# Kernel optimization log

Hardware: AMD Instinct MI355X
Metric: run time of the kernel (lower is better)

## Reference

```python
import jax, jax.numpy as jnp
import numpy as np

N = 100000      # nodes
E = 1600000     # edges (before self-loops)
FIN = 128       # in_channels
HID = 16        # hidden_channels
H = 8           # heads (layer 1)
OUT = 64        # out_channels
LN_EPS = 1e-5


def setup_inputs() -> dict:
    key = jax.random.key(0)
    ks = jax.random.split(key, 24)
    def p(i, shape):
        return jax.random.normal(ks[i], shape, dtype=jnp.float32) * 0.05
    return {
        "x": jax.random.normal(ks[0], (N, FIN), dtype=jnp.float32),
        "edge_index": jax.random.randint(ks[1], (2, E), 0, N, dtype=jnp.int32),
        # GATv2 layer 1: in -> H*HID, concat
        "Wl1": p(2, (FIN, H * HID)), "bl1": p(3, (H * HID,)),
        "Wr1": p(4, (FIN, H * HID)), "br1": p(5, (H * HID,)),
        "att1": p(6, (H, HID)), "bias1": p(7, (H * HID,)),
        # GATv2 layer 2: H*HID -> HID, heads=1
        "Wl2": p(8, (H * HID, HID)), "bl2": p(9, (HID,)),
        "Wr2": p(10, (H * HID, HID)), "br2": p(11, (HID,)),
        "att2": p(12, (1, HID)), "bias2": p(13, (HID,)),
        # LayerNorms
        "ln1_g": jnp.ones((H * HID,), jnp.float32), "ln1_b": jnp.zeros((H * HID,), jnp.float32),
        "ln2_g": jnp.ones((HID,), jnp.float32), "ln2_b": jnp.zeros((HID,), jnp.float32),
        # residual / skip / output linears
        "res1_W": p(14, (FIN, H * HID)), "res1_b": p(15, (H * HID,)),
        "res2_W": p(16, (H * HID, HID)), "res2_b": p(17, (HID,)),
        "skip_W": p(18, (H * HID, HID)), "skip_b": p(19, (HID,)),
        "out_W": p(20, (HID, OUT)), "out_b": p(21, (OUT,)),
    }


def _layernorm(x, g, b):
    mu = jnp.mean(x, axis=-1, keepdims=True)
    var = jnp.mean((x - mu) ** 2, axis=-1, keepdims=True)
    return (x - mu) * jax.lax.rsqrt(var + LN_EPS) * g + b


def _gatv2(x, src, dst, Wl, bl, Wr, br, att, bias, concat):
    # PyG GATv2Conv (share_weights=False, eval mode): message from src j to dst i
    Hh, C = att.shape
    n = x.shape[0]
    xl = (x @ Wl + bl).reshape(n, Hh, C)   # source-side transform
    xr = (x @ Wr + br).reshape(n, Hh, C)   # target-side transform
    m = xl[src] + xr[dst]                  # [E, H, C]
    e = jax.nn.leaky_relu(m, 0.2)
    alpha = jnp.einsum('ehc,hc->eh', e, att)          # [E, H]
    amax = jax.ops.segment_max(alpha, dst, num_segments=n)
    alpha = jnp.exp(alpha - amax[dst])
    denom = jax.ops.segment_sum(alpha, dst, num_segments=n)
    alpha = alpha / (denom[dst] + 1e-16)
    out = jax.ops.segment_sum(xl[src] * alpha[:, :, None], dst, num_segments=n)  # [N, H, C]
    out = out.reshape(n, Hh * C) if concat else out.mean(axis=1)
    return out + bias


def reference(x, edge_index, Wl1, bl1, Wr1, br1, att1, bias1,
              Wl2, bl2, Wr2, br2, att2, bias2,
              ln1_g, ln1_b, ln2_g, ln2_b,
              res1_W, res1_b, res2_W, res2_b, skip_W, skip_b, out_W, out_b):
    n = x.shape[0]
    loops = jnp.arange(n, dtype=edge_index.dtype)
    src = jnp.concatenate([edge_index[0], loops])
    dst = jnp.concatenate([edge_index[1], loops])

    h = _gatv2(x, src, dst, Wl1, bl1, Wr1, br1, att1, bias1, concat=True)
    h = _layernorm(h, ln1_g, ln1_b)
    h = h + (x @ res1_W + res1_b)
    h = jax.nn.elu(h)            # dropout off in eval

    skip_in = h
    h2 = _gatv2(h, src, dst, Wl2, bl2, Wr2, br2, att2, bias2, concat=False)
    h2 = _layernorm(h2, ln2_g, ln2_b)
    h2 = h2 + (skip_in @ res2_W + res2_b)
    h2 = jax.nn.elu(h2)
    h2 = h2 + (skip_in @ skip_W + skip_b)
    return h2 @ out_W + out_b
```

## Files before the change

### kernel.cpp

```cpp
#include <hip/hip_runtime.h>

typedef __attribute__((ext_vector_type(8))) short bf16x8;
typedef __attribute__((ext_vector_type(4))) float f32x4;

__device__ __forceinline__ float bf2f(ushort u) {
  union { uint i; float f; } v; v.i = ((uint)u) << 16; return v.f;
}
__device__ __forceinline__ ushort f2bf(float f) {
  union { float f; uint i; } v; v.f = f;
  uint r = (v.i + 0x7FFFu + ((v.i >> 16) & 1u)) >> 16;
  return (ushort)r;
}
__device__ __forceinline__ float blo(uint u) { return __builtin_bit_cast(float, u << 16); }
__device__ __forceinline__ float bhi(uint u) { return __builtin_bit_cast(float, u & 0xffff0000u); }

template <int CTRL>
__device__ __forceinline__ float dppadd(float x) {
  union { float f; int i; } a, b;
  a.f = x;
  b.i = __builtin_amdgcn_update_dpp(0, a.i, CTRL, 0xF, 0xF, true);
  return a.f + b.f;
}
#define DPP_X1 0xB1
#define DPP_X2 0x4E
#define DPP_X7 0x141
#define DPP_XF 0x140


__global__ __launch_bounds__(256) void k_init(
    const float* __restrict__ Wl1, const float* __restrict__ bl1,
    const float* __restrict__ Wr1, const float* __restrict__ br1,
    const float* __restrict__ res1W, const float* __restrict__ res1b,
    const float* __restrict__ Wl2, const float* __restrict__ bl2,
    const float* __restrict__ Wr2, const float* __restrict__ br2,
    const float* __restrict__ res2W, const float* __restrict__ res2b,
    const float* __restrict__ skipW, const float* __restrict__ skipb,
    const float* __restrict__ att1, const float* __restrict__ att2,
    ushort* __restrict__ W1F, float* __restrict__ B1P,
    ushort* __restrict__ W2F, float* __restrict__ B2P,
    float* __restrict__ at6, float* __restrict__ at4, float* __restrict__ at2E,
    int* __restrict__ cnt, int N) {
  const float LOG2E = 1.4426950408889634f;
  int b = blockIdx.x, t = threadIdx.x;
  if (b < 227) {
    int tid = b * 256 + t;
    if (tid < 49152) {
      int j = tid & 7, l = (tid >> 3) & 63, ktile = (tid >> 9) & 3, ct = tid >> 11;
      int k = ktile * 32 + ((l >> 4) << 3) + j;
      int n = ct * 16 + (l & 15);
      int sel = n >> 7, jj = n & 127;
      const float* s = sel == 0 ? Wl1 : sel == 1 ? Wr1 : res1W;
      W1F[tid] = f2bf(s[k * 128 + jj]);
    } else if (tid < 57344) {
      int u = tid - 49152;
      int j = u & 7, l = (u >> 3) & 63, ktile = (u >> 9) & 3, ct = u >> 11;
      int k = ktile * 32 + ((l >> 4) << 3) + j;
      int n = ct * 16 + (l & 15);
      int sel = n >> 4, jj = n & 15;
      const float* s = sel == 0 ? Wl2 : sel == 1 ? Wr2 : sel == 2 ? res2W : skipW;
      W2F[u] = f2bf(s[k * 16 + jj]);
    } else if (tid < 57728) {
      int n = tid - 57344;
      int sel = n >> 7, jj = n & 127;
      const float* sb = sel == 0 ? bl1 : sel == 1 ? br1 : res1b;
      B1P[n] = sb[jj];
    } else if (tid < 57792) {
      int n = tid - 57728;
      int sel = n >> 4, jj = n & 15;
      const float* sb = sel == 0 ? bl2 : sel == 1 ? br2 : sel == 2 ? res2b : skipb;
      B2P[n] = sb[jj];
    } else if (tid < 57920) {
      int n = tid - 57792;
      at6[n] = att1[n] * 0.6f * LOG2E;
    } else if (tid < 58048) {
      int n = tid - 57920;
      at4[n] = att1[n] * 0.4f * LOG2E;
    } else if (tid < 58064) {
      int n = tid - 58048;
      at2E[n] = att2[n] * LOG2E;
    }
  } else {
    int idx = (b - 227) * 256 + t;
    if (idx < N) cnt[idx] = 0;
  }
}


__global__ __launch_bounds__(256) void k_hist(const int* __restrict__ ei, int* __restrict__ cnt, int E) {
  int e4 = (blockIdx.x * 256 + threadIdx.x) * 4;
  if (e4 + 3 < E) {
    int4 d = *(const int4*)&ei[E + e4];
    atomicAdd(&cnt[d.x], 1); atomicAdd(&cnt[d.y], 1);
    atomicAdd(&cnt[d.z], 1); atomicAdd(&cnt[d.w], 1);
  } else {
    for (int e = e4; e < E; ++e) atomicAdd(&cnt[ei[E + e]], 1);
  }
}


__global__ __launch_bounds__(256) void k_scan1(const int* __restrict__ cnt, int* __restrict__ partial, int n) {
  int i = blockIdx.x * 256 + threadIdx.x;
  int v = (i < n) ? cnt[i] : 0;
  #pragma unroll
  for (int m = 1; m < 64; m <<= 1) v += __shfl_xor(v, m);
  __shared__ int sm[4];
  if ((threadIdx.x & 63) == 0) sm[threadIdx.x >> 6] = v;
  __syncthreads();
  if (threadIdx.x == 0) partial[blockIdx.x] = sm[0] + sm[1] + sm[2] + sm[3];
}


__global__ __launch_bounds__(256) void k_scan3lb(const int* __restrict__ cnt, const int* __restrict__ partial,
                                                 int* __restrict__ rowptr, int* __restrict__ cursor, int n) {
  int t = threadIdx.x;
  int b = blockIdx.x;
  int acc = 0;
  for (int j = t; j < b; j += 256) acc += partial[j];
  #pragma unroll
  for (int m = 1; m < 64; m <<= 1) acc += __shfl_xor(acc, m);
  __shared__ int sm[4];
  if ((t & 63) == 0) sm[t >> 6] = acc;
  __syncthreads();
  int base = sm[0] + sm[1] + sm[2] + sm[3];
  __shared__ int buf[2][256];
  int i = b * 256 + t;
  int v = (i < n) ? cnt[i] : 0;
  buf[0][t] = v;
  __syncthreads();
  int cur = 0;
  for (int off = 1; off < 256; off <<= 1) {
    int x = buf[cur][t];
    if (t >= off) x += buf[cur][t - off];
    buf[cur ^ 1][t] = x;
    __syncthreads();
    cur ^= 1;
  }
  if (i < n) {
    int incl = buf[cur][t];
    int rp = base + incl - v;
    rowptr[i] = rp;
    cursor[i] = rp;
    if (i == n - 1) rowptr[n] = base + incl;
  }
}


__global__ __launch_bounds__(256) void k_scatter(const int* __restrict__ ei, int* __restrict__ cursor,
                                                 int* __restrict__ ssrc, int E, int NS) {
  int t = threadIdx.x;
  int base = blockIdx.x * 2048;
  int src[8], dst[8];
  #pragma unroll
  for (int j = 0; j < 8; ++j) {
    int idx = base + j * 256 + t;
    bool ok = idx < E;
    src[j] = ok ? ei[idx] : 0;
    dst[j] = ok ? ei[E + idx] : -1;
  }
  for (int s = 0; s < NS; ++s) {
    #pragma unroll
    for (int j = 0; j < 8; ++j) {
      if ((dst[j] >> 13) == s) {
        int pos = atomicAdd(&cursor[dst[j]], 1);
        ssrc[pos] = src[j];
      }
    }
  }
}


__global__ __launch_bounds__(256) void k_gemm1(
    const float* __restrict__ x, const ushort* __restrict__ WF,
    const float* __restrict__ bias,
    ushort* __restrict__ O0, ushort* __restrict__ O1, ushort* __restrict__ O2,
    int M) {
  __shared__ ushort LT[64 * 392];
  int t = threadIdx.x, w = t >> 6, l = t & 63;
  int m0 = blockIdx.x * 64;
  int rql = l & 15, kq = l >> 4;
  bf16x8 afr[16];
  #pragma unroll
  for (int kt = 0; kt < 4; ++kt) {
    #pragma unroll
    for (int rt = 0; rt < 4; ++rt) {
      int m = m0 + rt * 16 + rql;
      uint4 o = make_uint4(0, 0, 0, 0);
      if (m < M) {
        const float* src = x + (size_t)m * 128 + kt * 32 + kq * 8;
        float4 f0 = *(const float4*)src;
        float4 f1 = *(const float4*)(src + 4);
        o.x = f2bf(f0.x) | ((uint)f2bf(f0.y) << 16);
        o.y = f2bf(f0.z) | ((uint)f2bf(f0.w) << 16);
        o.z = f2bf(f1.x) | ((uint)f2bf(f1.y) << 16);
        o.w = f2bf(f1.z) | ((uint)f2bf(f1.w) << 16);
      }
      afr[kt * 4 + rt] = __builtin_bit_cast(bf16x8, o);
    }
  }
  #pragma unroll
  for (int ct6 = 0; ct6 < 6; ++ct6) {
    int ct = w * 6 + ct6;
    int col = ct * 16 + rql;
    float bv = bias[col];
    f32x4 acc[4] = {};
    #pragma unroll
    for (int kt = 0; kt < 4; ++kt) {
      bf16x8 b = *(const bf16x8*)(WF + ((size_t)((ct * 4 + kt) * 64 + l)) * 8);
      #pragma unroll
      for (int rt = 0; rt < 4; ++rt)
        acc[rt] = __builtin_amdgcn_mfma_f32_16x16x32_bf16(afr[kt * 4 + rt], b, acc[rt], 0, 0, 0);
    }
    #pragma unroll
    for (int rt = 0; rt < 4; ++rt)
      #pragma unroll
      for (int r = 0; r < 4; ++r)
        LT[(rt * 16 + kq * 4 + r) * 392 + col] = f2bf(acc[rt][r] + bv);
  }
  __syncthreads();
  #pragma unroll
  for (int a = 0; a < 3; ++a) {
    ushort* O = a == 0 ? O0 : a == 1 ? O1 : O2;
    #pragma unroll
    for (int it = 0; it < 4; ++it) {
      int idx = it * 256 + t;
      int row = idx >> 4, seg = idx & 15;
      int m = m0 + row;
      if (m < M) {
        uint4 v = *(const uint4*)&LT[row * 392 + a * 128 + seg * 8];
        *(uint4*)&O[(size_t)m * 128 + seg * 8] = v;
      }
    }
  }
}


__global__ __launch_bounds__(256) void k_mfma2(
    const ushort* __restrict__ AF, const ushort* __restrict__ WF,
    const float* __restrict__ bias,
    ushort* __restrict__ O0, ushort* __restrict__ O1,
    ushort* __restrict__ O2, ushort* __restrict__ O3, int M) {
  int w = threadIdx.x >> 6, l = threadIdx.x & 63;
  int m0 = blockIdx.x * 64;
  int c0 = w * 16;
  int ct = c0 >> 4;
  f32x4 acc[4] = {};
  #pragma unroll
  for (int kt = 0; kt < 4; ++kt) {
    bf16x8 b = *(const bf16x8*)(WF + ((size_t)((ct * 4 + kt) * 64 + l)) * 8);
    #pragma unroll
    for (int rt = 0; rt < 4; ++rt) {
      bf16x8 a = *(const bf16x8*)(AF + ((size_t)((blockIdx.x * 16 + rt * 4 + kt) * 64 + l)) * 8);
      acc[rt] = __builtin_amdgcn_mfma_f32_16x16x32_bf16(a, b, acc[rt], 0, 0, 0);
    }
  }
  int col = c0 + (l & 15);
  int arr = col >> 4;
  ushort* O = arr == 0 ? O0 : arr == 1 ? O1 : arr == 2 ? O2 : O3;
  int lcol = col & 15;
  float bv = bias[col];
  int rbase = m0 + ((l >> 4) << 2);
  #pragma unroll
  for (int rt = 0; rt < 4; ++rt) {
    #pragma unroll
    for (int r = 0; r < 4; ++r) {
      int m = rbase + rt * 16 + r;
      if (m < M) O[(size_t)m * 16 + lcol] = f2bf(acc[rt][r] + bv);
    }
  }
}


#define EDGE1B(u, MASKHI)                                              \
  {                                                                    \
    float v0 = blo((u).x), v1 = bhi((u).x);                            \
    float v2 = blo((u).y), v3 = bhi((u).y);                            \
    float m0 = v0 + xr0, m1 = v1 + xr1, m2 = v2 + xr2, m3 = v3 + xr3;  \
    float d = a6.x * m0 + a4.x * __builtin_fabsf(m0);                  \
    d += a6.y * m1; d += a4.y * __builtin_fabsf(m1);                   \
    d += a6.z * m2; d += a4.z * __builtin_fabsf(m2);                   \
    d += a6.w * m3; d += a4.w * __builtin_fabsf(m3);                   \
    d = dppadd<DPP_X1>(d);                                             \
    d = dppadd<DPP_X2>(d);                                             \
    float p = __builtin_amdgcn_exp2f(d);                               \
    if (MASKHI) p = hi ? 0.f : p;                                      \
    acc0 += p * v0; acc1 += p * v1; acc2 += p * v2; acc3 += p * v3;    \
    den += p;                                                          \
  }

__global__ __launch_bounds__(256) void k_gat1(
    const ushort* __restrict__ XLG, const ushort* __restrict__ XR,
    const ushort* __restrict__ RE,
    const float* __restrict__ at6, const float* __restrict__ at4,
    const float* __restrict__ bias1,
    const float* __restrict__ g1, const float* __restrict__ b1,
    const int* __restrict__ rowptr, const int* __restrict__ ssrc,
    ushort* __restrict__ HF, int n) {
  int lane = threadIdx.x & 63;
  int i = blockIdx.x * 4 + (threadIdx.x >> 6);
  if (i >= n) return;
  int l32 = lane & 31;
  bool hi = lane >= 32;
  int fb = l32 * 4;
  size_t rowb = (size_t)i << 8;
  uint2 uxr = *(const uint2*)((const char*)XR + rowb + (fb << 1));
  float xr0 = blo(uxr.x), xr1 = bhi(uxr.x), xr2 = blo(uxr.y), xr3 = bhi(uxr.y);
  float4 a6 = *(const float4*)&at6[fb];
  float4 a4 = *(const float4*)&at4[fb];
  float acc0 = 0.f, acc1 = 0.f, acc2 = 0.f, acc3 = 0.f, den = 0.f;
  {
    uint2 us = *(const uint2*)((const char*)XLG + rowb + (fb << 1));
    EDGE1B(us, true);
  }
  int e0 = __builtin_amdgcn_readfirstlane(rowptr[i]);
  int e1 = __builtin_amdgcn_readfirstlane(rowptr[i + 1]);
  for (int base = e0; base < e1; base += 64) {
    int cnt = e1 - base; if (cnt > 64) cnt = 64;
    int sidx = ssrc[base + (lane < cnt ? lane : cnt - 1)];
    int j = 0;
    for (; j + 4 <= cnt; j += 4) {
      int s0 = __builtin_amdgcn_readlane(sidx, j);
      int s1 = __builtin_amdgcn_readlane(sidx, j + 1);
      int s2 = __builtin_amdgcn_readlane(sidx, j + 2);
      int s3 = __builtin_amdgcn_readlane(sidx, j + 3);
      int rA = hi ? s1 : s0;
      int rB = hi ? s3 : s2;
      uint2 uA = *(const uint2*)((const char*)XLG + ((size_t)(uint)rA << 8) + (fb << 1));
      uint2 uB = *(const uint2*)((const char*)XLG + ((size_t)(uint)rB << 8) + (fb << 1));
      EDGE1B(uA, false);
      EDGE1B(uB, false);
    }
    for (; j + 2 <= cnt; j += 2) {
      int s0 = __builtin_amdgcn_readlane(sidx, j);
      int s1 = __builtin_amdgcn_readlane(sidx, j + 1);
      int r = hi ? s1 : s0;
      uint2 u = *(const uint2*)((const char*)XLG + ((size_t)(uint)r << 8) + (fb << 1));
      EDGE1B(u, false);
    }
    if (j < cnt) {
      int s0 = __builtin_amdgcn_readlane(sidx, j);
      uint2 u = *(const uint2*)((const char*)XLG + ((size_t)(uint)s0 << 8) + (fb << 1));
      EDGE1B(u, true);
    }
  }
  acc0 += __shfl_xor(acc0, 32);
  acc1 += __shfl_xor(acc1, 32);
  acc2 += __shfl_xor(acc2, 32);
  acc3 += __shfl_xor(acc3, 32);
  den  += __shfl_xor(den, 32);
  float inv = 1.f / (den + 1e-16f);
  float4 bv = *(const float4*)&bias1[fb];
  float o0 = acc0 * inv + bv.x, o1 = acc1 * inv + bv.y;
  float o2 = acc2 * inv + bv.z, o3 = acc3 * inv + bv.w;
  float s = o0 + o1 + o2 + o3;
  #pragma unroll
  for (int m = 1; m < 32; m <<= 1) s += __shfl_xor(s, m);
  float mu = s * (1.f / 128.f);
  float d0 = o0 - mu, d1 = o1 - mu, d2 = o2 - mu, d3 = o3 - mu;
  float q = d0 * d0 + d1 * d1 + d2 * d2 + d3 * d3;
  #pragma unroll
  for (int m = 1; m < 32; m <<= 1) q += __shfl_xor(q, m);
  float rstd = rsqrtf(q * (1.f / 128.f) + 1e-5f);
  float4 gg = *(const float4*)&g1[fb];
  float4 bb = *(const float4*)&b1[fb];
  uint2 ur = *(const uint2*)((const char*)RE + rowb + (fb << 1));
  float r0 = blo(ur.x), r1 = bhi(ur.x), r2 = blo(ur.y), r3 = bhi(ur.y);
  float y0 = d0 * rstd * gg.x + bb.x + r0;
  float y1 = d1 * rstd * gg.y + bb.y + r1;
  float y2 = d2 * rstd * gg.z + bb.z + r2;
  float y3 = d3 * rstd * gg.w + bb.w + r3;
  y0 = y0 > 0.f ? y0 : __expf(y0) - 1.f;
  y1 = y1 > 0.f ? y1 : __expf(y1) - 1.f;
  y2 = y2 > 0.f ? y2 : __expf(y2) - 1.f;
  y3 = y3 > 0.f ? y3 : __expf(y3) - 1.f;
  if (!hi) {
    int k8 = l32 >> 1;
    size_t slot = ((size_t)(i >> 4) * 4 + (k8 >> 2)) * 64 + (i & 15) + ((k8 & 3) << 4);
    uint2 o;
    o.x = (uint)f2bf(y0) | ((uint)f2bf(y1) << 16);
    o.y = (uint)f2bf(y2) | ((uint)f2bf(y3) << 16);
    *(uint2*)(HF + slot * 8 + (l32 & 1) * 4) = o;
  }
}


#define EDGE2V(v)                                            \
  {                                                          \
    float m = (v) + xr;                                      \
    float ta = a2 * m;                                       \
    float tb = a2 * __builtin_fabsf(m);                      \
    float tt = 0.6f * ta + 0.4f * tb;                        \
    tt = dppadd<DPP_X1>(tt);                                 \
    tt = dppadd<DPP_X2>(tt);                                 \
    tt = dppadd<DPP_X7>(tt);                                 \
    tt = dppadd<DPP_XF>(tt);                                 \
    float p = __builtin_amdgcn_exp2f(tt);                    \
    acc += p * (v); den += p;                                \
  }

__global__ __launch_bounds__(256) void k_gat2(
    const ushort* __restrict__ XG, const ushort* __restrict__ XRr,
    const ushort* __restrict__ XE, const ushort* __restrict__ XS,
    const float* __restrict__ at2E, const float* __restrict__ bias2,
    const float* __restrict__ g2, const float* __restrict__ b2,
    const int* __restrict__ rowptr, const int* __restrict__ ssrc,
    const float* __restrict__ outW, const float* __restrict__ outB,
    float* __restrict__ Out, int n) {
  __shared__ float sW[1024];
  __shared__ float sB[64];
  int t = threadIdx.x;
  for (int idx = t; idx < 1024; idx += 256) sW[idx] = outW[idx];
  if (t < 64) sB[t] = outB[t];
  __syncthreads();
  int c = t & 15;
  int i = blockIdx.x * 16 + (t >> 4);
  if (i >= n) return;
  size_t ib = (size_t)i << 4;
  float xl = bf2f(XG[ib + c]), xr = bf2f(XRr[ib + c]);
  float resv = bf2f(XE[ib + c]), skipv = bf2f(XS[ib + c]);
  float a2 = at2E[c];
  float acc = 0.f, den = 0.f;
  EDGE2V(xl);
  int e0 = rowptr[i], e1 = rowptr[i + 1];
  int e = e0;
  for (; e + 4 <= e1; e += 4) {
    int s0 = ssrc[e], s1 = ssrc[e + 1], s2 = ssrc[e + 2], s3 = ssrc[e + 3];
    float v0 = bf2f(XG[((size_t)(uint)s0 << 4) + c]);
    float v1 = bf2f(XG[((size_t)(uint)s1 << 4) + c]);
    float v2 = bf2f(XG[((size_t)(uint)s2 << 4) + c]);
    float v3 = bf2f(XG[((size_t)(uint)s3 << 4) + c]);
    EDGE2V(v0); EDGE2V(v1); EDGE2V(v2); EDGE2V(v3);
  }
  for (; e < e1; ++e) {
    int s = ssrc[e];
    float v = bf2f(XG[((size_t)(uint)s << 4) + c]);
    EDGE2V(v);
  }
  float o = acc / (den + 1e-16f) + bias2[c];
  float s = o;
  s = dppadd<DPP_X1>(s); s = dppadd<DPP_X2>(s); s = dppadd<DPP_X7>(s); s = dppadd<DPP_XF>(s);
  float mu = s * (1.f / 16.f);
  float d = o - mu;
  float q = d * d;
  q = dppadd<DPP_X1>(q); q = dppadd<DPP_X2>(q); q = dppadd<DPP_X7>(q); q = dppadd<DPP_XF>(q);
  float rstd = rsqrtf(q * (1.f / 16.f) + 1e-5f);
  float y = d * rstd * g2[c] + b2[c] + resv;
  y = y > 0.f ? y : __expf(y) - 1.f;
  y += skipv;
  float a0 = sB[c * 4 + 0], a1 = sB[c * 4 + 1], ao2 = sB[c * 4 + 2], a3 = sB[c * 4 + 3];
  #pragma unroll
  for (int cc = 0; cc < 16; ++cc) {
    float h = __shfl(y, cc, 16);
    a0 += h * sW[cc * 64 + c * 4 + 0];
    a1 += h * sW[cc * 64 + c * 4 + 1];
    ao2 += h * sW[cc * 64 + c * 4 + 2];
    a3 += h * sW[cc * 64 + c * 4 + 3];
  }
  *(float4*)&Out[(size_t)i * 64 + c * 4] = make_float4(a0, a1, ao2, a3);
}


extern "C" void kernel_launch(void* const* d_in, const int* in_sizes, int n_in,
                              void* d_out, int out_size, void* d_ws, size_t ws_size,
                              hipStream_t stream) {
  const float* x     = (const float*)d_in[0];
  const int*   ei    = (const int*)d_in[1];
  const float* Wl1   = (const float*)d_in[2];
  const float* bl1   = (const float*)d_in[3];
  const float* Wr1   = (const float*)d_in[4];
  const float* br1   = (const float*)d_in[5];
  const float* att1  = (const float*)d_in[6];
  const float* bias1 = (const float*)d_in[7];
  const float* Wl2   = (const float*)d_in[8];
  const float* bl2   = (const float*)d_in[9];
  const float* Wr2   = (const float*)d_in[10];
  const float* br2   = (const float*)d_in[11];
  const float* att2  = (const float*)d_in[12];
  const float* bias2 = (const float*)d_in[13];
  const float* ln1g  = (const float*)d_in[14];
  const float* ln1b  = (const float*)d_in[15];
  const float* ln2g  = (const float*)d_in[16];
  const float* ln2b  = (const float*)d_in[17];
  const float* res1W = (const float*)d_in[18];
  const float* res1b = (const float*)d_in[19];
  const float* res2W = (const float*)d_in[20];
  const float* res2b = (const float*)d_in[21];
  const float* skipW = (const float*)d_in[22];
  const float* skipb = (const float*)d_in[23];
  const float* outW  = (const float*)d_in[24];
  const float* outb  = (const float*)d_in[25];
  int N = in_sizes[0] / 128;
  int E = in_sizes[1] / 2;
  float* out = (float*)d_out;

  int nblk = (N + 63) / 64;
  int ngrp = nblk * 4;

  ushort* XLG  = (ushort*)d_ws;
  ushort* XR1  = XLG + (size_t)N * 128;
  ushort* RE1  = XR1 + (size_t)N * 128;
  ushort* HF   = RE1 + (size_t)N * 128;
  ushort* XG2  = HF + (size_t)ngrp * 2048;
  ushort* X2R  = XG2 + (size_t)N * 16;
  ushort* X2E  = X2R + (size_t)N * 16;
  ushort* X2S  = X2E + (size_t)N * 16;
  ushort* W1F  = X2S + (size_t)N * 16;
  ushort* W2F  = W1F + 49152;
  float*  B1P  = (float*)(W2F + 8192);
  float*  B2P  = B1P + 384;
  float*  at6  = B2P + 64;
  float*  at4  = at6 + 128;
  float*  at2E = at4 + 128;
  int* cnt     = (int*)(at2E + 16);
  int* cursor  = cnt + N;
  int* rowptr  = cursor + N;
  int* ssrc    = rowptr + N + 1;
  int* partial = ssrc + E;

  int nbS = (N + 255) / 256;
  int NS  = ((N - 1) >> 13) + 1;
  int nScat = (E + 2047) / 2048;

  k_init<<<227 + nbS, 256, 0, stream>>>(Wl1, bl1, Wr1, br1, res1W, res1b,
                                        Wl2, bl2, Wr2, br2, res2W, res2b, skipW, skipb,
                                        att1, att2, W1F, B1P, W2F, B2P, at6, at4, at2E,
                                        cnt, N);
  k_hist<<<(E + 1023) / 1024, 256, 0, stream>>>(ei, cnt, E);
  k_scan1<<<nbS, 256, 0, stream>>>(cnt, partial, N);
  k_scan3lb<<<nbS, 256, 0, stream>>>(cnt, partial, rowptr, cursor, N);
  k_scatter<<<nScat, 256, 0, stream>>>(ei, cursor, ssrc, E, NS);
  k_gemm1<<<nblk, 256, 0, stream>>>(x, W1F, B1P, XLG, XR1, RE1, N);
  k_gat1<<<(N + 3) / 4, 256, 0, stream>>>(XLG, XR1, RE1, at6, at4, bias1, ln1g, ln1b,
                                          rowptr, ssrc, HF, N);
  k_mfma2<<<nblk, 256, 0, stream>>>(HF, W2F, B2P, XG2, X2R, X2E, X2S, N);
  k_gat2<<<(N + 15) / 16, 256, 0, stream>>>(XG2, X2R, X2E, X2S, at2E, bias2, ln2g, ln2b,
                                            rowptr, ssrc, outW, outb, out, N);
}
```

Measured before the change: 472.9 us.

## Fuse histogram with layer-1 GEMM launch, use bpermute gathers, unroll gat2

Merges the degree histogram kernel and the layer-1 MFMA GEMM into one launch, with block ranges split by role, so both run concurrently and one launch is removed. In gat1, per-edge source indices are broadcast with ds_bpermute (each half-wave gets its own edge) instead of readlane plus select, and the inner loop handles 8 edges per iteration. gat2's edge loop is unrolled from 4 to 8 to keep more gathers in flight. The fused kernel gives histogram blocks the GEMM's large shared-memory allocation, which can limit occupancy, and the 32-bit byte offset for gathers assumes the XLG buffer stays under 4 GB.

Result: no change. 466.2 us (-1.4%).

```diff
diff --git a/kernel.cpp b/kernel.cpp
--- a/kernel.cpp
+++ b/kernel.cpp
@@ -86,14 +86,80 @@
 }
 
 
-__global__ __launch_bounds__(256) void k_hist(const int* __restrict__ ei, int* __restrict__ cnt, int E) {
-  int e4 = (blockIdx.x * 256 + threadIdx.x) * 4;
-  if (e4 + 3 < E) {
-    int4 d = *(const int4*)&ei[E + e4];
-    atomicAdd(&cnt[d.x], 1); atomicAdd(&cnt[d.y], 1);
-    atomicAdd(&cnt[d.z], 1); atomicAdd(&cnt[d.w], 1);
-  } else {
-    for (int e = e4; e < E; ++e) atomicAdd(&cnt[ei[E + e]], 1);
+__global__ __launch_bounds__(256) void k_histgemm(
+    const int* __restrict__ ei, int* __restrict__ cnt, int E, int nh,
+    const float* __restrict__ x, const ushort* __restrict__ WF,
+    const float* __restrict__ bias,
+    ushort* __restrict__ O0, ushort* __restrict__ O1, ushort* __restrict__ O2,
+    int M) {
+  __shared__ ushort LT[64 * 392];
+  int b = blockIdx.x, t = threadIdx.x;
+  if (b < nh) {
+    int e4 = (b * 256 + t) * 4;
+    if (e4 + 3 < E) {
+      int4 d = *(const int4*)&ei[E + e4];
+      atomicAdd(&cnt[d.x], 1); atomicAdd(&cnt[d.y], 1);
+      atomicAdd(&cnt[d.z], 1); atomicAdd(&cnt[d.w], 1);
+    } else {
+      for (int e = e4; e < E; ++e) atomicAdd(&cnt[ei[E + e]], 1);
+    }
+    return;
+  }
+  int w = t >> 6, l = t & 63;
+  int m0 = (b - nh) * 64;
+  int rql = l & 15, kq = l >> 4;
+  bf16x8 afr[16];
+  #pragma unroll
+  for (int kt = 0; kt < 4; ++kt) {
+    #pragma unroll
+    for (int rt = 0; rt < 4; ++rt) {
+      int m = m0 + rt * 16 + rql;
+      uint4 o = make_uint4(0, 0, 0, 0);
+      if (m < M) {
+        const float* src = x + (size_t)m * 128 + kt * 32 + kq * 8;
+        float4 f0 = *(const float4*)src;
+        float4 f1 = *(const float4*)(src + 4);
+        o.x = f2bf(f0.x) | ((uint)f2bf(f0.y) << 16);
+        o.y = f2bf(f0.z) | ((uint)f2bf(f0.w) << 16);
+        o.z = f2bf(f1.x) | ((uint)f2bf(f1.y) << 16);
+        o.w = f2bf(f1.z) | ((uint)f2bf(f1.w) << 16);
+      }
+      afr[kt * 4 + rt] = __builtin_bit_cast(bf16x8, o);
+    }
+  }
+  #pragma unroll
+  for (int ct6 = 0; ct6 < 6; ++ct6) {
+    int ct = w * 6 + ct6;
+    int col = ct * 16 + rql;
+    float bv = bias[col];
+    f32x4 acc[4] = {};
+    #pragma unroll
+    for (int kt = 0; kt < 4; ++kt) {
+      bf16x8 bfrag = *(const bf16x8*)(WF + ((size_t)((ct * 4 + kt) * 64 + l)) * 8);
+      #pragma unroll
+      for (int rt = 0; rt < 4; ++rt)
+        acc[rt] = __builtin_amdgcn_mfma_f32_16x16x32_bf16(afr[kt * 4 + rt], bfrag, acc[rt], 0, 0, 0);
+    }
+    #pragma unroll
+    for (int rt = 0; rt < 4; ++rt)
+      #pragma unroll
+      for (int r = 0; r < 4; ++r)
+        LT[(rt * 16 + kq * 4 + r) * 392 + col] = f2bf(acc[rt][r] + bv);
+  }
+  __syncthreads();
+  #pragma unroll
+  for (int a = 0; a < 3; ++a) {
+    ushort* O = a == 0 ? O0 : a == 1 ? O1 : O2;
+    #pragma unroll
+    for (int it = 0; it < 4; ++it) {
+      int idx = it * 256 + t;
+      int row = idx >> 4, seg = idx & 15;
+      int m = m0 + row;
+      if (m < M) {
+        uint4 v = *(const uint4*)&LT[row * 392 + a * 128 + seg * 8];
+        *(uint4*)&O[(size_t)m * 128 + seg * 8] = v;
+      }
+    }
   }
 }
 
@@ -169,71 +235,6 @@
 }
 
 
-__global__ __launch_bounds__(256) void k_gemm1(
-    const float* __restrict__ x, const ushort* __restrict__ WF,
-    const float* __restrict__ bias,
-    ushort* __restrict__ O0, ushort* __restrict__ O1, ushort* __restrict__ O2,
-    int M) {
-  __shared__ ushort LT[64 * 392];
-  int t = threadIdx.x, w = t >> 6, l = t & 63;
-  int m0 = blockIdx.x * 64;
-  int rql = l & 15, kq = l >> 4;
-  bf16x8 afr[16];
-  #pragma unroll
-  for (int kt = 0; kt < 4; ++kt) {
-    #pragma unroll
-    for (int rt = 0; rt < 4; ++rt) {
-      int m = m0 + rt * 16 + rql;
-      uint4 o = make_uint4(0, 0, 0, 0);
-      if (m < M) {
-        const float* src = x + (size_t)m * 128 + kt * 32 + kq * 8;
-        float4 f0 = *(const float4*)src;
-        float4 f1 = *(const float4*)(src + 4);
-        o.x = f2bf(f0.x) | ((uint)f2bf(f0.y) << 16);
-        o.y = f2bf(f0.z) | ((uint)f2bf(f0.w) << 16);
-        o.z = f2bf(f1.x) | ((uint)f2bf(f1.y) << 16);
-        o.w = f2bf(f1.z) | ((uint)f2bf(f1.w) << 16);
-      }
-      afr[kt * 4 + rt] = __builtin_bit_cast(bf16x8, o);
-    }
-  }
-  #pragma unroll
-  for (int ct6 = 0; ct6 < 6; ++ct6) {
-    int ct = w * 6 + ct6;
-    int col = ct * 16 + rql;
-    float bv = bias[col];
-    f32x4 acc[4] = {};
-    #pragma unroll
-    for (int kt = 0; kt < 4; ++kt) {
-      bf16x8 b = *(const bf16x8*)(WF + ((size_t)((ct * 4 + kt) * 64 + l)) * 8);
-      #pragma unroll
-      for (int rt = 0; rt < 4; ++rt)
-        acc[rt] = __builtin_amdgcn_mfma_f32_16x16x32_bf16(afr[kt * 4 + rt], b, acc[rt], 0, 0, 0);
-    }
-    #pragma unroll
-    for (int rt = 0; rt < 4; ++rt)
-      #pragma unroll
-      for (int r = 0; r < 4; ++r)
-        LT[(rt * 16 + kq * 4 + r) * 392 + col] = f2bf(acc[rt][r] + bv);
-  }
-  __syncthreads();
-  #pragma unroll
-  for (int a = 0; a < 3; ++a) {
-    ushort* O = a == 0 ? O0 : a == 1 ? O1 : O2;
-    #pragma unroll
-    for (int it = 0; it < 4; ++it) {
-      int idx = it * 256 + t;
-      int row = idx >> 4, seg = idx & 15;
-      int m = m0 + row;
-      if (m < M) {
-        uint4 v = *(const uint4*)&LT[row * 392 + a * 128 + seg * 8];
-        *(uint4*)&O[(size_t)m * 128 + seg * 8] = v;
-      }
-    }
-  }
-}
-
-
 __global__ __launch_bounds__(256) void k_mfma2(
     const ushort* __restrict__ AF, const ushort* __restrict__ WF,
     const float* __restrict__ bias,
@@ -300,15 +301,17 @@
   if (i >= n) return;
   int l32 = lane & 31;
   bool hi = lane >= 32;
+  int hioff4 = (lane & 32) >> 3;
+  int fbb = l32 << 3;
   int fb = l32 * 4;
   size_t rowb = (size_t)i << 8;
-  uint2 uxr = *(const uint2*)((const char*)XR + rowb + (fb << 1));
+  uint2 uxr = *(const uint2*)((const char*)XR + rowb + fbb);
   float xr0 = blo(uxr.x), xr1 = bhi(uxr.x), xr2 = blo(uxr.y), xr3 = bhi(uxr.y);
   float4 a6 = *(const float4*)&at6[fb];
   float4 a4 = *(const float4*)&at4[fb];
   float acc0 = 0.f, acc1 = 0.f, acc2 = 0.f, acc3 = 0.f, den = 0.f;
   {
-    uint2 us = *(const uint2*)((const char*)XLG + rowb + (fb << 1));
+    uint2 us = *(const uint2*)((const char*)XLG + rowb + fbb);
     EDGE1B(us, true);
   }
   int e0 = __builtin_amdgcn_readfirstlane(rowptr[i]);
@@ -317,28 +320,25 @@
     int cnt = e1 - base; if (cnt > 64) cnt = 64;
     int sidx = ssrc[base + (lane < cnt ? lane : cnt - 1)];
     int j = 0;
-    for (; j + 4 <= cnt; j += 4) {
-      int s0 = __builtin_amdgcn_readlane(sidx, j);
-      int s1 = __builtin_amdgcn_readlane(sidx, j + 1);
-      int s2 = __builtin_amdgcn_readlane(sidx, j + 2);
-      int s3 = __builtin_amdgcn_readlane(sidx, j + 3);
-      int rA = hi ? s1 : s0;
-      int rB = hi ? s3 : s2;
-      uint2 uA = *(const uint2*)((const char*)XLG + ((size_t)(uint)rA << 8) + (fb << 1));
-      uint2 uB = *(const uint2*)((const char*)XLG + ((size_t)(uint)rB << 8) + (fb << 1));
-      EDGE1B(uA, false);
-      EDGE1B(uB, false);
+    for (; j + 8 <= cnt; j += 8) {
+      uint o0 = (uint)__builtin_amdgcn_ds_bpermute(((j + 0) << 2) + hioff4, sidx) << 8;
+      uint o1 = (uint)__builtin_amdgcn_ds_bpermute(((j + 2) << 2) + hioff4, sidx) << 8;
+      uint o2 = (uint)__builtin_amdgcn_ds_bpermute(((j + 4) << 2) + hioff4, sidx) << 8;
+      uint o3 = (uint)__builtin_amdgcn_ds_bpermute(((j + 6) << 2) + hioff4, sidx) << 8;
+      uint2 u0 = *(const uint2*)((const char*)XLG + o0 + fbb);
+      uint2 u1 = *(const uint2*)((const char*)XLG + o1 + fbb);
+      uint2 u2 = *(const uint2*)((const char*)XLG + o2 + fbb);
+      uint2 u3 = *(const uint2*)((const char*)XLG + o3 + fbb);
+      EDGE1B(u0, false); EDGE1B(u1, false); EDGE1B(u2, false); EDGE1B(u3, false);
     }
     for (; j + 2 <= cnt; j += 2) {
-      int s0 = __builtin_amdgcn_readlane(sidx, j);
-      int s1 = __builtin_amdgcn_readlane(sidx, j + 1);
-      int r = hi ? s1 : s0;
-      uint2 u = *(const uint2*)((const char*)XLG + ((size_t)(uint)r << 8) + (fb << 1));
+      uint o = (uint)__builtin_amdgcn_ds_bpermute((j << 2) + hioff4, sidx) << 8;
+      uint2 u = *(const uint2*)((const char*)XLG + o + fbb);
       EDGE1B(u, false);
     }
     if (j < cnt) {
-      int s0 = __builtin_amdgcn_readlane(sidx, j);
-      uint2 u = *(const uint2*)((const char*)XLG + ((size_t)(uint)s0 << 8) + (fb << 1));
+      uint o = (uint)__builtin_amdgcn_ds_bpermute((j << 2) + hioff4, sidx) << 8;
+      uint2 u = *(const uint2*)((const char*)XLG + o + fbb);
       EDGE1B(u, true);
     }
   }
@@ -362,7 +362,7 @@
   float rstd = rsqrtf(q * (1.f / 128.f) + 1e-5f);
   float4 gg = *(const float4*)&g1[fb];
   float4 bb = *(const float4*)&b1[fb];
-  uint2 ur = *(const uint2*)((const char*)RE + rowb + (fb << 1));
+  uint2 ur = *(const uint2*)((const char*)RE + rowb + fbb);
   float r0 = blo(ur.x), r1 = bhi(ur.x), r2 = blo(ur.y), r3 = bhi(ur.y);
   float y0 = d0 * rstd * gg.x + bb.x + r0;
   float y1 = d1 * rstd * gg.y + bb.y + r1;
@@ -422,13 +422,19 @@
   EDGE2V(xl);
   int e0 = rowptr[i], e1 = rowptr[i + 1];
   int e = e0;
-  for (; e + 4 <= e1; e += 4) {
-    int s0 = ssrc[e], s1 = ssrc[e + 1], s2 = ssrc[e + 2], s3 = ssrc[e + 3];
+  for (; e + 8 <= e1; e += 8) {
+    int s0 = ssrc[e],     s1 = ssrc[e + 1], s2 = ssrc[e + 2], s3 = ssrc[e + 3];
+    int s4 = ssrc[e + 4], s5 = ssrc[e + 5], s6 = ssrc[e + 6], s7 = ssrc[e + 7];
     float v0 = bf2f(XG[((size_t)(uint)s0 << 4) + c]);
     float v1 = bf2f(XG[((size_t)(uint)s1 << 4) + c]);
     float v2 = bf2f(XG[((size_t)(uint)s2 << 4) + c]);
     float v3 = bf2f(XG[((size_t)(uint)s3 << 4) + c]);
+    float v4 = bf2f(XG[((size_t)(uint)s4 << 4) + c]);
+    float v5 = bf2f(XG[((size_t)(uint)s5 << 4) + c]);
+    float v6 = bf2f(XG[((size_t)(uint)s6 << 4) + c]);
+    float v7 = bf2f(XG[((size_t)(uint)s7 << 4) + c]);
     EDGE2V(v0); EDGE2V(v1); EDGE2V(v2); EDGE2V(v3);
+    EDGE2V(v4); EDGE2V(v5); EDGE2V(v6); EDGE2V(v7);
   }
   for (; e < e1; ++e) {
     int s = ssrc[e];
@@ -519,16 +525,17 @@
   int nbS = (N + 255) / 256;
   int NS  = ((N - 1) >> 13) + 1;
   int nScat = (E + 2047) / 2048;
+  int nh = (E + 1023) / 1024;
 
   k_init<<<227 + nbS, 256, 0, stream>>>(Wl1, bl1, Wr1, br1, res1W, res1b,
                                         Wl2, bl2, Wr2, br2, res2W, res2b, skipW, skipb,
                                         att1, att2, W1F, B1P, W2F, B2P, at6, at4, at2E,
                                         cnt, N);
-  k_hist<<<(E + 1023) / 1024, 256, 0, stream>>>(ei, cnt, E);
+  k_histgemm<<<nh + nblk, 256, 0, stream>>>(ei, cnt, E, nh, x, W1F, B1P,
+                                            XLG, XR1, RE1, N);
   k_scan1<<<nbS, 256, 0, stream>>>(cnt, partial, N);
   k_scan3lb<<<nbS, 256, 0, stream>>>(cnt, partial, rowptr, cursor, N);
   k_scatter<<<nScat, 256, 0, stream>>>(ei, cursor, ssrc, E, NS);
-  k_gemm1<<<nblk, 256, 0, stream>>>(x, W1F, B1P, XLG, XR1, RE1, N);
   k_gat1<<<(N + 3) / 4, 256, 0, stream>>>(XLG, XR1, RE1, at6, at4, bias1, ln1g, ln1b,
                                           rowptr, ssrc, HF, N);
   k_mfma2<<<nblk, 256, 0, stream>>>(HF, W2F, B2P, XG2, X2R, X2E, X2S, N);
```
